# Kernel tuning notes

Measured on AMD Instinct MI355X. Metric: run time of the kernel, lower is better.

The kernel has to match this reference:

```python
import jax, jax.numpy as jnp
import numpy as np

H, D_MODEL, DK, DV = 16, 1024, 64, 64
B, S = 4, 2048
LN_EPS = 1e-6
NEG = -1e9


def setup_inputs() -> dict:
    key = jax.random.key(0)
    ks = jax.random.split(key, 8)
    query = jax.random.normal(ks[0], (B, S, D_MODEL), dtype=jnp.float32)
    k_in = jax.random.normal(ks[1], (B, S, D_MODEL), dtype=jnp.float32)
    v_in = jax.random.normal(ks[2], (B, S, D_MODEL), dtype=jnp.float32)
    mask = jax.random.randint(ks[3], (B, S, S), 0, 2, dtype=jnp.int32)
    sc = 1.0 / np.sqrt(D_MODEL)
    w_qs = jax.random.normal(ks[4], (D_MODEL, H * DK), dtype=jnp.float32) * sc
    w_ks = jax.random.normal(ks[5], (D_MODEL, H * DK), dtype=jnp.float32) * sc
    w_vs = jax.random.normal(ks[6], (D_MODEL, H * DV), dtype=jnp.float32) * sc
    w_out = jax.random.normal(ks[7], (H * DV, D_MODEL), dtype=jnp.float32) * (1.0 / np.sqrt(H * DV))
    ln_g = jnp.ones((D_MODEL,), dtype=jnp.float32)
    ln_b = jnp.zeros((D_MODEL,), dtype=jnp.float32)
    return {"query": query, "key": k_in, "value": v_in, "mask": mask,
            "w_qs": w_qs, "w_ks": w_ks, "w_vs": w_vs, "w_out": w_out,
            "ln_g": ln_g, "ln_b": ln_b}


def reference(query, key, value, mask, w_qs, w_ks, w_vs, w_out, ln_g, ln_b):
    # projections -> [B, H, S, dk/dv]
    q = (query @ w_qs).reshape(B, S, H, DK).transpose(0, 2, 1, 3)
    k = (key @ w_ks).reshape(B, S, H, DK).transpose(0, 2, 1, 3)
    v = (value @ w_vs).reshape(B, S, H, DV).transpose(0, 2, 1, 3)
    scores = jnp.einsum('bhqd,bhkd->bhqk', q, k) / np.sqrt(DK)
    scores = jnp.where(mask[:, None, :, :] == 0, NEG, scores)
    p = jax.nn.softmax(scores, axis=-1)  # dropout = identity in eval
    x = jnp.einsum('bhqk,bhkd->bhqd', p, v)  # [B,H,S,DV]
    x = x.transpose(0, 2, 1, 3).reshape(B, S, H * DV)
    out = x @ w_out + query  # dropout identity, residual
    mu = out.mean(-1, keepdims=True)
    var = out.var(-1, keepdims=True)
    return (out - mu) / jnp.sqrt(var + LN_EPS) * ln_g + ln_b
```

## Files before the change

### kernel.cpp

```cpp
#include <hip/hip_runtime.h>

#define BB   4
#define SS   2048
#define HH   16
#define DM   1024
#define DKV  64
#define LNEPS 1e-6f

#define MD_BF16 0
#define MD_F32  1
#define MD_F16  2

typedef __attribute__((ext_vector_type(8))) short bf16x8;
typedef __attribute__((ext_vector_type(4))) float f32x4;
#define MFMA16(a,b,c) __builtin_amdgcn_mfma_f32_16x16x32_bf16(a,b,c,0,0,0)

__device__ __forceinline__ void gl_lds16(const ushort* g, ushort* l) {
    __builtin_amdgcn_global_load_lds(
        (const __attribute__((address_space(1))) void*)g,
        (__attribute__((address_space(3))) void*)l, 16, 0, 0);
}

__device__ __forceinline__ float2 unpack2(unsigned int u) {
    union { unsigned int i; float f; } a, b;
    a.i = u << 16;
    b.i = u & 0xffff0000u;
    return make_float2(a.f, b.f);
}
__device__ __forceinline__ unsigned short f2bf(float f) {
    union { float f; unsigned int i; } c; c.f = f;
    unsigned int u = c.i;
    unsigned int r = u + 0x7fffu + ((u >> 16) & 1u);
    return (unsigned short)(r >> 16);
}
__device__ __forceinline__ unsigned short f2bf_t(float f) {
    union { float f; unsigned int i; } c; c.f = f;
    return (unsigned short)(c.i >> 16);
}
__device__ __forceinline__ float h2f(unsigned int bits16) {
    unsigned short s = (unsigned short)bits16;
    _Float16 x;
    __builtin_memcpy(&x, &s, 2);
    return (float)x;
}
__device__ __forceinline__ void load8m(const void* p, int mode, size_t e0, float* o) {
    if (mode == MD_F32) {
        const float* f = (const float*)p + e0;
        float4 a = *(const float4*)f;
        float4 b = *(const float4*)(f + 4);
        o[0] = a.x; o[1] = a.y; o[2] = a.z; o[3] = a.w;
        o[4] = b.x; o[5] = b.y; o[6] = b.z; o[7] = b.w;
    } else {
        uint4 u = *(const uint4*)((const ushort*)p + e0);
        unsigned v[4] = {u.x, u.y, u.z, u.w};
        if (mode == MD_BF16) {
#pragma unroll
            for (int j = 0; j < 4; ++j) { float2 t = unpack2(v[j]); o[2*j] = t.x; o[2*j+1] = t.y; }
        } else {
#pragma unroll
            for (int j = 0; j < 4; ++j) { o[2*j] = h2f(v[j] & 0xFFFFu); o[2*j+1] = h2f(v[j] >> 16); }
        }
    }
}
__device__ __forceinline__ void load4m(const void* p, int mode, size_t e0, float* o) {
    if (mode == MD_F32) {
        float4 v = *(const float4*)((const float*)p + e0);
        o[0] = v.x; o[1] = v.y; o[2] = v.z; o[3] = v.w;
    } else {
        uint2 u = *(const uint2*)((const ushort*)p + e0);
        if (mode == MD_BF16) {
            float2 a = unpack2(u.x), b = unpack2(u.y);
            o[0] = a.x; o[1] = a.y; o[2] = b.x; o[3] = b.y;
        } else {
            o[0] = h2f(u.x & 0xFFFFu); o[1] = h2f(u.x >> 16);
            o[2] = h2f(u.y & 0xFFFFu); o[3] = h2f(u.y >> 16);
        }
    }
}
__device__ __forceinline__ float loadS(const void* p, int mode, size_t i) {
    if (mode == MD_F32) return ((const float*)p)[i];
    unsigned short u = ((const ushort*)p)[i];
    if (mode == MD_BF16) { union { unsigned i; float f; } c; c.i = (unsigned)u << 16; return c.f; }
    return h2f(u);
}

struct SniffArgs { const void* p[10]; int nhalf[10]; };

__global__ void sniff_all(SniffArgs a, int* __restrict__ modes) {
    __shared__ int cE, cO;
    const int slots[9] = {0, 1, 2, 4, 5, 6, 7, 8, 9};
    const int slot = slots[blockIdx.x];
    const ushort* p = (const ushort*)a.p[slot];
    const int nhalf = a.nhalf[slot];
    if (threadIdx.x == 0) { cE = 0; cO = 0; }
    __syncthreads();
    int e = 0, o = 0;
    for (int i = threadIdx.x; i < nhalf; i += 256) {
        unsigned ex = (p[i] >> 7) & 0xFFu;
        int hit = (ex < 100u || ex == 0xFFu) ? 1 : 0;
        if (i & 1) o += hit; else e += hit;
    }
    atomicAdd(&cE, e);
    atomicAdd(&cO, o);
    __syncthreads();
    if (threadIdx.x == 0) {
        int total = cE + cO;
        modes[slot] = (total < 48) ? MD_BF16 : ((cO * 4 < cE) ? MD_F32 : MD_F16);
    }
}

__global__ __launch_bounds__(256) void mpack(
    const int* __restrict__ mask, unsigned int* __restrict__ pm)
{
    const int w = blockIdx.x * 256 + threadIdx.x;
    const int* p = mask + (size_t)w * 32;
    unsigned int bits = 0u;
#pragma unroll
    for (int j = 0; j < 8; ++j) {
        int4 v = *(const int4*)(p + j * 4);
        bits |= (v.x ? 1u : 0u) << (4 * j);
        bits |= (v.y ? 1u : 0u) << (4 * j + 1);
        bits |= (v.z ? 1u : 0u) << (4 * j + 2);
        bits |= (v.w ? 1u : 0u) << (4 * j + 3);
    }
    pm[w] = bits;
}

__global__ __launch_bounds__(256) void aconv(
    const void* __restrict__ A, ushort* __restrict__ Ab,
    const int* __restrict__ modes, int slot)
{
    const int m = modes[slot];
    const size_t e0 = ((size_t)blockIdx.x * 256 + threadIdx.x) * 16;
    float t[16];
    load8m(A, m, e0, t);
    load8m(A, m, e0 + 8, t + 8);
    union { ushort u[16]; uint4 v[2]; } p;
#pragma unroll
    for (int j = 0; j < 16; ++j) p.u[j] = f2bf(t[j]);
    *(uint4*)&Ab[e0]     = p.v[0];
    *(uint4*)&Ab[e0 + 8] = p.v[1];
}

__global__ __launch_bounds__(256) void wtrans(
    const void* __restrict__ W, ushort* __restrict__ Wt,
    const int* __restrict__ modes, int wslot)
{
    __shared__ ushort T[64][68];
    const int tid = threadIdx.x;
    const int m = modes[wslot];
    const int k0 = blockIdx.y * 64, n0 = blockIdx.x * 64;

    const int r = tid >> 2, c = (tid & 3) * 16;
    float t[4];
#pragma unroll
    for (int j = 0; j < 4; ++j) {
        load4m(W, m, (size_t)(k0 + r) * DM + n0 + c + 4 * j, t);
#pragma unroll
        for (int i = 0; i < 4; ++i) T[r][c + 4 * j + i] = f2bf(t[i]);
    }
    __syncthreads();

    const int rn = tid >> 2, ck = (tid & 3) * 16;
    union { ushort u[8]; uint4 v; } p0, p1;
#pragma unroll
    for (int j = 0; j < 8; ++j) { p0.u[j] = T[ck + j][rn]; p1.u[j] = T[ck + 8 + j][rn]; }
    ushort* op = &Wt[(size_t)(n0 + rn) * DM + k0 + ck];
    *(uint4*)op = p0.v;
    *(uint4*)(op + 8) = p1.v;
}

__global__ __launch_bounds__(256) void proj_mfma(
    const ushort* __restrict__ A, const ushort* __restrict__ Wt,
    ushort* __restrict__ Out, int vmode, float scale)
{
    __shared__ __align__(16) ushort Asf[128 * 32];
    __shared__ __align__(16) ushort Bsf[128 * 32];

    const int tid = threadIdx.x;
    const int lane = tid & 63, wv = tid >> 6;
    const int quad = lane >> 4, L = lane & 15;
    const int m0 = blockIdx.y * 128, n0 = blockIdx.x * 128;
    const int wm = (wv >> 1) * 64, wn = (wv & 1) * 64;

    const int e0 = (wv * 2 + 0) * 512 + lane * 8;
    const int e1 = (wv * 2 + 1) * 512 + lane * 8;
    const ushort* gA0 = A  + (size_t)(m0 + (e0 >> 5)) * DM + (e0 & 31);
    const ushort* gA1 = A  + (size_t)(m0 + (e1 >> 5)) * DM + (e1 & 31);
    const ushort* gB0 = Wt + (size_t)(n0 + (e0 >> 5)) * DM + (e0 & 31);
    const ushort* gB1 = Wt + (size_t)(n0 + (e1 >> 5)) * DM + (e1 & 31);

    f32x4 acc[4][4];
#pragma unroll
    for (int i = 0; i < 4; ++i)
#pragma unroll
        for (int j = 0; j < 4; ++j) { acc[i][j][0] = 0.f; acc[i][j][1] = 0.f; acc[i][j][2] = 0.f; acc[i][j][3] = 0.f; }

    for (int kt = 0; kt < 32; ++kt) {
        const int k0 = kt * 32;
        gl_lds16(gA0 + k0, &Asf[e0]);
        gl_lds16(gA1 + k0, &Asf[e1]);
        gl_lds16(gB0 + k0, &Bsf[e0]);
        gl_lds16(gB1 + k0, &Bsf[e1]);
        __syncthreads();

        bf16x8 af[4], bfr[4];
#pragma unroll
        for (int tm = 0; tm < 4; ++tm) af[tm] = *(const bf16x8*)&Asf[(wm + tm * 16 + L) * 32 + quad * 8];
#pragma unroll
        for (int tn = 0; tn < 4; ++tn) bfr[tn] = *(const bf16x8*)&Bsf[(wn + tn * 16 + L) * 32 + quad * 8];
#pragma unroll
        for (int tm = 0; tm < 4; ++tm)
#pragma unroll
            for (int tn = 0; tn < 4; ++tn)
                acc[tm][tn] = MFMA16(af[tm], bfr[tn], acc[tm][tn]);
        __syncthreads();
    }

#pragma unroll
    for (int tm = 0; tm < 4; ++tm)
#pragma unroll
        for (int tn = 0; tn < 4; ++tn)
#pragma unroll
            for (int r = 0; r < 4; ++r) {
                const int mm = m0 + wm + tm * 16 + quad * 4 + r;
                const int n = n0 + wn + tn * 16 + L;
                const int b = mm >> 11, s = mm & 2047;
                const int h = n >> 6, d = n & 63;
                const size_t o = vmode
                    ? ((size_t)(b * HH + h) * DKV + d) * SS + s
                    : ((size_t)(b * HH + h) * SS + s) * DKV + d;
                Out[o] = f2bf(acc[tm][tn][r] * scale);
            }
}

__global__ __launch_bounds__(256) void attn_mfma(
    const ushort* __restrict__ Q, const ushort* __restrict__ K,
    const ushort* __restrict__ Vt, const unsigned int* __restrict__ pm,
    ushort* __restrict__ Xo)
{
    __shared__ __align__(16) ushort Ks[64][72];
    __shared__ __align__(16) ushort Vs[64][72];
    __shared__ __align__(16) ushort Ps[64][72];

    const int tid = threadIdx.x;
    const int lane = tid & 63, wv = tid >> 6;
    const int quad = lane >> 4, L = lane & 15;
    const int bh = blockIdx.y, b = bh >> 4, h = bh & 15;
    const int q0 = blockIdx.x * 64;

    const ushort* qp = &Q[((size_t)bh * SS + q0 + wv * 16 + L) * DKV + quad * 8];
    const bf16x8 aq0 = *(const bf16x8*)qp;
    const bf16x8 aq1 = *(const bf16x8*)(qp + 32);

    f32x4 O[4];
    float lacc[4];
#pragma unroll
    for (int t = 0; t < 4; ++t) { O[t][0] = 0.f; O[t][1] = 0.f; O[t][2] = 0.f; O[t][3] = 0.f; }
#pragma unroll
    for (int r = 0; r < 4; ++r) lacc[r] = 0.f;

    const int sr = tid >> 2, sg = tid & 3;
    const ushort* kbase = &K[((size_t)bh * SS + sr) * DKV + sg * 16];
    const ushort* vbase = &Vt[((size_t)bh * DKV + sr) * SS + sg * 16];
    const unsigned int* pmr[4];
#pragma unroll
    for (int r = 0; r < 4; ++r)
        pmr[r] = pm + ((size_t)b * SS + q0 + wv * 16 + quad * 4 + r) * 64;

    for (int kt = 0; kt < 32; ++kt) {
        __syncthreads();
        *(uint4*)&Ks[sr][sg * 16]     = *(const uint4*)kbase;
        *(uint4*)&Ks[sr][sg * 16 + 8] = *(const uint4*)(kbase + 8);
        *(uint4*)&Vs[sr][sg * 16]     = *(const uint4*)vbase;
        *(uint4*)&Vs[sr][sg * 16 + 8] = *(const uint4*)(vbase + 8);
        kbase += 64 * DKV;
        vbase += 64;

        uint2 mw[4];
#pragma unroll
        for (int r = 0; r < 4; ++r) mw[r] = *(const uint2*)(pmr[r] + 2 * kt);

        __syncthreads();

        f32x4 sc[4];
#pragma unroll
        for (int t = 0; t < 4; ++t) {
            bf16x8 b0 = *(const bf16x8*)&Ks[t * 16 + L][quad * 8];
            bf16x8 b1 = *(const bf16x8*)&Ks[t * 16 + L][32 + quad * 8];
            f32x4 c; c[0] = 0.f; c[1] = 0.f; c[2] = 0.f; c[3] = 0.f;
            c = MFMA16(aq0, b0, c);
            c = MFMA16(aq1, b1, c);
            sc[t] = c;
        }

#pragma unroll
        for (int r = 0; r < 4; ++r) {
            const unsigned mx = mw[r].x, my = mw[r].y;
#pragma unroll
            for (int t = 0; t < 4; ++t) {
                const float s = fminf(sc[t][r], 30.f);
                const float e = __expf(s);
                const unsigned wsel = (t & 2) ? my : mx;
                const float p = ((wsel >> ((t & 1) * 16 + L)) & 1u) ? e : 0.f;
                lacc[r] += p;
                Ps[wv * 16 + quad * 4 + r][t * 16 + L] = f2bf_t(p);
            }
        }

        bf16x8 ap0 = *(const bf16x8*)&Ps[wv * 16 + L][quad * 8];
        bf16x8 ap1 = *(const bf16x8*)&Ps[wv * 16 + L][32 + quad * 8];
#pragma unroll
        for (int t = 0; t < 4; ++t) {
            bf16x8 v0 = *(const bf16x8*)&Vs[t * 16 + L][quad * 8];
            bf16x8 v1 = *(const bf16x8*)&Vs[t * 16 + L][32 + quad * 8];
            O[t] = MFMA16(ap0, v0, O[t]);
            O[t] = MFMA16(ap1, v1, O[t]);
        }
    }

    float inv[4];
#pragma unroll
    for (int r = 0; r < 4; ++r) {
        float l = lacc[r];
#pragma unroll
        for (int off = 1; off < 16; off <<= 1) l += __shfl_xor(l, off, 64);
        inv[r] = 1.f / l;
    }
#pragma unroll
    for (int t = 0; t < 4; ++t)
#pragma unroll
        for (int r = 0; r < 4; ++r) {
            const int qg = q0 + wv * 16 + quad * 4 + r;
            Xo[((size_t)b * SS + qg) * DM + h * DKV + t * 16 + L] = f2bf(O[t][r] * inv[r]);
        }
}

__global__ __launch_bounds__(256) void oproj_mfma(
    const ushort* __restrict__ Xin, const ushort* __restrict__ Wt,
    const void* __restrict__ Qres, float* __restrict__ Out,
    const int* __restrict__ modes)
{
    __shared__ __align__(16) ushort Asf[128 * 32];
    __shared__ __align__(16) ushort Bsf[128 * 32];

    const int tid = threadIdx.x;
    const int lane = tid & 63, wv = tid >> 6;
    const int quad = lane >> 4, L = lane & 15;
    const int m0 = blockIdx.y * 128, n0 = blockIdx.x * 128;
    const int wm = (wv >> 1) * 64, wn = (wv & 1) * 64;
    const int mq = modes[0];

    const int e0 = (wv * 2 + 0) * 512 + lane * 8;
    const int e1 = (wv * 2 + 1) * 512 + lane * 8;
    const ushort* gA0 = Xin + (size_t)(m0 + (e0 >> 5)) * DM + (e0 & 31);
    const ushort* gA1 = Xin + (size_t)(m0 + (e1 >> 5)) * DM + (e1 & 31);
    const ushort* gB0 = Wt  + (size_t)(n0 + (e0 >> 5)) * DM + (e0 & 31);
    const ushort* gB1 = Wt  + (size_t)(n0 + (e1 >> 5)) * DM + (e1 & 31);

    f32x4 acc[4][4];
#pragma unroll
    for (int i = 0; i < 4; ++i)
#pragma unroll
        for (int j = 0; j < 4; ++j) { acc[i][j][0] = 0.f; acc[i][j][1] = 0.f; acc[i][j][2] = 0.f; acc[i][j][3] = 0.f; }

    for (int kt = 0; kt < 32; ++kt) {
        const int k0 = kt * 32;
        gl_lds16(gA0 + k0, &Asf[e0]);
        gl_lds16(gA1 + k0, &Asf[e1]);
        gl_lds16(gB0 + k0, &Bsf[e0]);
        gl_lds16(gB1 + k0, &Bsf[e1]);
        __syncthreads();

        bf16x8 af[4], bfr[4];
#pragma unroll
        for (int tm = 0; tm < 4; ++tm) af[tm] = *(const bf16x8*)&Asf[(wm + tm * 16 + L) * 32 + quad * 8];
#pragma unroll
        for (int tn = 0; tn < 4; ++tn) bfr[tn] = *(const bf16x8*)&Bsf[(wn + tn * 16 + L) * 32 + quad * 8];
#pragma unroll
        for (int tm = 0; tm < 4; ++tm)
#pragma unroll
            for (int tn = 0; tn < 4; ++tn)
                acc[tm][tn] = MFMA16(af[tm], bfr[tn], acc[tm][tn]);
        __syncthreads();
    }

#pragma unroll
    for (int tm = 0; tm < 4; ++tm)
#pragma unroll
        for (int tn = 0; tn < 4; ++tn)
#pragma unroll
            for (int r = 0; r < 4; ++r) {
                const int mm = m0 + wm + tm * 16 + quad * 4 + r;
                const int n = n0 + wn + tn * 16 + L;
                const size_t idx = (size_t)mm * DM + n;
                Out[idx] = acc[tm][tn][r] + loadS(Qres, mq, idx);
            }
}

__global__ __launch_bounds__(256) void ln_k(
    float* __restrict__ Out, const void* __restrict__ G,
    const void* __restrict__ Bt, const int* __restrict__ modes)
{
    const int tid = threadIdx.x, wv = tid >> 6, lane = tid & 63;
    const int row = blockIdx.x * 4 + wv;
    const int mg = modes[8], mb = modes[9];
    const size_t base = (size_t)row * DM + lane * 16;

    float v[16];
    float s = 0.f, q = 0.f;
#pragma unroll
    for (int j = 0; j < 16; j += 4) {
        float4 t = *(const float4*)&Out[base + j];
        v[j] = t.x; v[j+1] = t.y; v[j+2] = t.z; v[j+3] = t.w;
        s += t.x + t.y + t.z + t.w;
        q += t.x*t.x + t.y*t.y + t.z*t.z + t.w*t.w;
    }
#pragma unroll
    for (int off = 1; off < 64; off <<= 1) {
        s += __shfl_xor(s, off, 64);
        q += __shfl_xor(q, off, 64);
    }
    const float mu = s * (1.f / 1024.f);
    const float var = q * (1.f / 1024.f) - mu * mu;
    const float inv = rsqrtf(var + LNEPS);

    float gj[16], bj[16];
#pragma unroll
    for (int j = 0; j < 16; j += 4) {
        load4m(G,  mg, (size_t)lane * 16 + j, gj + j);
        load4m(Bt, mb, (size_t)lane * 16 + j, bj + j);
    }
#pragma unroll
    for (int j = 0; j < 16; j += 4) {
        float4 o;
        o.x = (v[j]   - mu) * inv * gj[j]   + bj[j];
        o.y = (v[j+1] - mu) * inv * gj[j+1] + bj[j+1];
        o.z = (v[j+2] - mu) * inv * gj[j+2] + bj[j+2];
        o.w = (v[j+3] - mu) * inv * gj[j+3] + bj[j+3];
        *(float4*)&Out[base + j] = o;
    }
}

extern "C" void kernel_launch(void* const* d_in, const int* in_sizes, int n_in,
                              void* d_out, int out_size, void* d_ws, size_t ws_size,
                              hipStream_t stream)
{
    const void* query = d_in[0];
    const void* key_i = d_in[1];
    const void* value = d_in[2];
    const int*  mask  = (const int*)d_in[3];
    const void* w_qs  = d_in[4];
    const void* w_ks  = d_in[5];
    const void* w_vs  = d_in[6];
    const void* w_out = d_in[7];
    const void* ln_g  = d_in[8];
    const void* ln_b  = d_in[9];
    float* out = (float*)d_out;

    int* modes = (int*)d_ws;
    const size_t PE = (size_t)BB * HH * SS * DKV;
    ushort* Qw = (ushort*)((char*)d_ws + 256);
    ushort* Kw = Qw + PE;
    ushort* Vw = Kw + PE;
    ushort* Xw = Vw + PE;
    ushort* Abuf = Xw;
    ushort* Wt   = (ushort*)((char*)d_out + (4 << 20));
    ushort* Wt2  = Qw;
    unsigned int* pmask = (unsigned int*)d_out;

    SniffArgs sa;
    for (int i = 0; i < 10; ++i) {
        sa.p[i] = d_in[i];
        sa.nhalf[i] = in_sizes[i] < 4096 ? in_sizes[i] : 4096;
    }
    sniff_all<<<9, 256, 0, stream>>>(sa, modes);
    mpack<<<2048, 256, 0, stream>>>(mask, pmask);

    dim3 gproj(8, 64), gtr(16, 16);

    wtrans<<<gtr, 256, 0, stream>>>(w_qs, Wt, modes, 4);
    aconv<<<2048, 256, 0, stream>>>(query, Abuf, modes, 0);
    proj_mfma<<<gproj, 256, 0, stream>>>(Abuf, Wt, Qw, 0, 0.125f);

    wtrans<<<gtr, 256, 0, stream>>>(w_ks, Wt, modes, 5);
    aconv<<<2048, 256, 0, stream>>>(key_i, Abuf, modes, 1);
    proj_mfma<<<gproj, 256, 0, stream>>>(Abuf, Wt, Kw, 0, 1.0f);

    wtrans<<<gtr, 256, 0, stream>>>(w_vs, Wt, modes, 6);
    aconv<<<2048, 256, 0, stream>>>(value, Abuf, modes, 2);
    proj_mfma<<<gproj, 256, 0, stream>>>(Abuf, Wt, Vw, 1, 1.0f);

    attn_mfma<<<dim3(32, 64), 256, 0, stream>>>(Qw, Kw, Vw, pmask, Xw);

    wtrans<<<gtr, 256, 0, stream>>>(w_out, Wt2, modes, 7);
    oproj_mfma<<<gproj, 256, 0, stream>>>(Xw, Wt2, query, out, modes);
    ln_k<<<2048, 256, 0, stream>>>(out, ln_g, ln_b, modes);
}
```

Measured before the change: 536.4 us.

## Double-buffer GEMM LDS loads, swizzle block order, batch weight transposes, set MFMA priority

The projection and output GEMMs now use double-buffered LDS tiles. The next k-slice's global_load_lds is issued before the MFMAs on the current slice, and each step ends with a single vmcnt wait plus barrier. This is meant to hide global-load latency. Block indices are swizzled in the GEMMs and in attention, so consecutive blocks share tiles in L2. The three QKV weight transposes are merged into one launch writing separate buffers, and s_setprio is raised around the MFMA sections in attention. The cost is double the LDS per GEMM block, which may reduce occupancy.

```diff
diff --git a/kernel.cpp b/kernel.cpp
--- a/kernel.cpp
+++ b/kernel.cpp
@@ -19,6 +19,10 @@
     __builtin_amdgcn_global_load_lds(
         (const __attribute__((address_space(1))) void*)g,
         (__attribute__((address_space(3))) void*)l, 16, 0, 0);
+}
+__device__ __forceinline__ void wait_vm0_barrier() {
+    asm volatile("s_waitcnt vmcnt(0)" ::: "memory");
+    __builtin_amdgcn_s_barrier();
 }
 
 __device__ __forceinline__ float2 unpack2(unsigned int u) {
@@ -142,13 +146,13 @@
     *(uint4*)&Ab[e0 + 8] = p.v[1];
 }
 
-__global__ __launch_bounds__(256) void wtrans(
-    const void* __restrict__ W, ushort* __restrict__ Wt,
-    const int* __restrict__ modes, int wslot)
+struct WtArgs { const void* W[3]; ushort* Wt[3]; int slot[3]; };
+
+__device__ __forceinline__ void wtrans_body(
+    const void* __restrict__ W, ushort* __restrict__ Wt, int m)
 {
     __shared__ ushort T[64][68];
     const int tid = threadIdx.x;
-    const int m = modes[wslot];
     const int k0 = blockIdx.y * 64, n0 = blockIdx.x * 64;
 
     const int r = tid >> 2, c = (tid & 3) * 16;
@@ -170,17 +174,30 @@
     *(uint4*)(op + 8) = p1.v;
 }
 
+__global__ __launch_bounds__(256) void wtrans3(WtArgs a, const int* __restrict__ modes) {
+    const int g = blockIdx.z;
+    wtrans_body(a.W[g], a.Wt[g], modes[a.slot[g]]);
+}
+__global__ __launch_bounds__(256) void wtrans(
+    const void* __restrict__ W, ushort* __restrict__ Wt,
+    const int* __restrict__ modes, int wslot)
+{
+    wtrans_body(W, Wt, modes[wslot]);
+}
+
 __global__ __launch_bounds__(256) void proj_mfma(
     const ushort* __restrict__ A, const ushort* __restrict__ Wt,
     ushort* __restrict__ Out, int vmode, float scale)
 {
-    __shared__ __align__(16) ushort Asf[128 * 32];
-    __shared__ __align__(16) ushort Bsf[128 * 32];
+    __shared__ __align__(16) ushort Asf[2][4096];
+    __shared__ __align__(16) ushort Bsf[2][4096];
 
     const int tid = threadIdx.x;
     const int lane = tid & 63, wv = tid >> 6;
     const int quad = lane >> 4, L = lane & 15;
-    const int m0 = blockIdx.y * 128, n0 = blockIdx.x * 128;
+    const int bid = blockIdx.y * gridDim.x + blockIdx.x;
+    const int swz = (bid & 7) * 64 + (bid >> 3);
+    const int m0 = (swz >> 3) * 128, n0 = (swz & 7) * 128;
     const int wm = (wv >> 1) * 64, wn = (wv & 1) * 64;
 
     const int e0 = (wv * 2 + 0) * 512 + lane * 8;
@@ -196,25 +213,45 @@
 #pragma unroll
         for (int j = 0; j < 4; ++j) { acc[i][j][0] = 0.f; acc[i][j][1] = 0.f; acc[i][j][2] = 0.f; acc[i][j][3] = 0.f; }
 
-    for (int kt = 0; kt < 32; ++kt) {
-        const int k0 = kt * 32;
-        gl_lds16(gA0 + k0, &Asf[e0]);
-        gl_lds16(gA1 + k0, &Asf[e1]);
-        gl_lds16(gB0 + k0, &Bsf[e0]);
-        gl_lds16(gB1 + k0, &Bsf[e1]);
-        __syncthreads();
+    gl_lds16(gA0, &Asf[0][e0]);
+    gl_lds16(gA1, &Asf[0][e1]);
+    gl_lds16(gB0, &Bsf[0][e0]);
+    gl_lds16(gB1, &Bsf[0][e1]);
+    wait_vm0_barrier();
+
+    int cur = 0;
+    for (int kt = 0; kt < 31; ++kt) {
+        const int kn = (kt + 1) * 32;
+        gl_lds16(gA0 + kn, &Asf[cur ^ 1][e0]);
+        gl_lds16(gA1 + kn, &Asf[cur ^ 1][e1]);
+        gl_lds16(gB0 + kn, &Bsf[cur ^ 1][e0]);
+        gl_lds16(gB1 + kn, &Bsf[cur ^ 1][e1]);
 
         bf16x8 af[4], bfr[4];
 #pragma unroll
-        for (int tm = 0; tm < 4; ++tm) af[tm] = *(const bf16x8*)&Asf[(wm + tm * 16 + L) * 32 + quad * 8];
-#pragma unroll
-        for (int tn = 0; tn < 4; ++tn) bfr[tn] = *(const bf16x8*)&Bsf[(wn + tn * 16 + L) * 32 + quad * 8];
+        for (int tm = 0; tm < 4; ++tm) af[tm] = *(const bf16x8*)&Asf[cur][(wm + tm * 16 + L) * 32 + quad * 8];
+#pragma unroll
+        for (int tn = 0; tn < 4; ++tn) bfr[tn] = *(const bf16x8*)&Bsf[cur][(wn + tn * 16 + L) * 32 + quad * 8];
 #pragma unroll
         for (int tm = 0; tm < 4; ++tm)
 #pragma unroll
             for (int tn = 0; tn < 4; ++tn)
                 acc[tm][tn] = MFMA16(af[tm], bfr[tn], acc[tm][tn]);
-        __syncthreads();
+
+        wait_vm0_barrier();
+        cur ^= 1;
+    }
+    {
+        bf16x8 af[4], bfr[4];
+#pragma unroll
+        for (int tm = 0; tm < 4; ++tm) af[tm] = *(const bf16x8*)&Asf[cur][(wm + tm * 16 + L) * 32 + quad * 8];
+#pragma unroll
+        for (int tn = 0; tn < 4; ++tn) bfr[tn] = *(const bf16x8*)&Bsf[cur][(wn + tn * 16 + L) * 32 + quad * 8];
+#pragma unroll
+        for (int tm = 0; tm < 4; ++tm)
+#pragma unroll
+            for (int tn = 0; tn < 4; ++tn)
+                acc[tm][tn] = MFMA16(af[tm], bfr[tn], acc[tm][tn]);
     }
 
 #pragma unroll
@@ -246,8 +283,10 @@
     const int tid = threadIdx.x;
     const int lane = tid & 63, wv = tid >> 6;
     const int quad = lane >> 4, L = lane & 15;
-    const int bh = blockIdx.y, b = bh >> 4, h = bh & 15;
-    const int q0 = blockIdx.x * 64;
+    const int bid = blockIdx.y * gridDim.x + blockIdx.x;
+    const int swz = (bid & 7) * 256 + (bid >> 3);
+    const int bh = swz >> 5, b = bh >> 4, h = bh & 15;
+    const int q0 = (swz & 31) * 64;
 
     const ushort* qp = &Q[((size_t)bh * SS + q0 + wv * 16 + L) * DKV + quad * 8];
     const bf16x8 aq0 = *(const bf16x8*)qp;
@@ -284,6 +323,7 @@
         __syncthreads();
 
         f32x4 sc[4];
+        __builtin_amdgcn_s_setprio(1);
 #pragma unroll
         for (int t = 0; t < 4; ++t) {
             bf16x8 b0 = *(const bf16x8*)&Ks[t * 16 + L][quad * 8];
@@ -293,6 +333,7 @@
             c = MFMA16(aq1, b1, c);
             sc[t] = c;
         }
+        __builtin_amdgcn_s_setprio(0);
 
 #pragma unroll
         for (int r = 0; r < 4; ++r) {
@@ -310,6 +351,7 @@
 
         bf16x8 ap0 = *(const bf16x8*)&Ps[wv * 16 + L][quad * 8];
         bf16x8 ap1 = *(const bf16x8*)&Ps[wv * 16 + L][32 + quad * 8];
+        __builtin_amdgcn_s_setprio(1);
 #pragma unroll
         for (int t = 0; t < 4; ++t) {
             bf16x8 v0 = *(const bf16x8*)&Vs[t * 16 + L][quad * 8];
@@ -317,6 +359,7 @@
             O[t] = MFMA16(ap0, v0, O[t]);
             O[t] = MFMA16(ap1, v1, O[t]);
         }
+        __builtin_amdgcn_s_setprio(0);
     }
 
     float inv[4];
@@ -341,13 +384,15 @@
     const void* __restrict__ Qres, float* __restrict__ Out,
     const int* __restrict__ modes)
 {
-    __shared__ __align__(16) ushort Asf[128 * 32];
-    __shared__ __align__(16) ushort Bsf[128 * 32];
+    __shared__ __align__(16) ushort Asf[2][4096];
+    __shared__ __align__(16) ushort Bsf[2][4096];
 
     const int tid = threadIdx.x;
     const int lane = tid & 63, wv = tid >> 6;
     const int quad = lane >> 4, L = lane & 15;
-    const int m0 = blockIdx.y * 128, n0 = blockIdx.x * 128;
+    const int bid = blockIdx.y * gridDim.x + blockIdx.x;
+    const int swz = (bid & 7) * 64 + (bid >> 3);
+    const int m0 = (swz >> 3) * 128, n0 = (swz & 7) * 128;
     const int wm = (wv >> 1) * 64, wn = (wv & 1) * 64;
     const int mq = modes[0];
 
@@ -364,25 +409,45 @@
 #pragma unroll
         for (int j = 0; j < 4; ++j) { acc[i][j][0] = 0.f; acc[i][j][1] = 0.f; acc[i][j][2] = 0.f; acc[i][j][3] = 0.f; }
 
-    for (int kt = 0; kt < 32; ++kt) {
-        const int k0 = kt * 32;
-        gl_lds16(gA0 + k0, &Asf[e0]);
-        gl_lds16(gA1 + k0, &Asf[e1]);
-        gl_lds16(gB0 + k0, &Bsf[e0]);
-        gl_lds16(gB1 + k0, &Bsf[e1]);
-        __syncthreads();
+    gl_lds16(gA0, &Asf[0][e0]);
+    gl_lds16(gA1, &Asf[0][e1]);
+    gl_lds16(gB0, &Bsf[0][e0]);
+    gl_lds16(gB1, &Bsf[0][e1]);
+    wait_vm0_barrier();
+
+    int cur = 0;
+    for (int kt = 0; kt < 31; ++kt) {
+        const int kn = (kt + 1) * 32;
+        gl_lds16(gA0 + kn, &Asf[cur ^ 1][e0]);
+        gl_lds16(gA1 + kn, &Asf[cur ^ 1][e1]);
+        gl_lds16(gB0 + kn, &Bsf[cur ^ 1][e0]);
+        gl_lds16(gB1 + kn, &Bsf[cur ^ 1][e1]);
 
         bf16x8 af[4], bfr[4];
 #pragma unroll
-        for (int tm = 0; tm < 4; ++tm) af[tm] = *(const bf16x8*)&Asf[(wm + tm * 16 + L) * 32 + quad * 8];
-#pragma unroll
-        for (int tn = 0; tn < 4; ++tn) bfr[tn] = *(const bf16x8*)&Bsf[(wn + tn * 16 + L) * 32 + quad * 8];
+        for (int tm = 0; tm < 4; ++tm) af[tm] = *(const bf16x8*)&Asf[cur][(wm + tm * 16 + L) * 32 + quad * 8];
+#pragma unroll
+        for (int tn = 0; tn < 4; ++tn) bfr[tn] = *(const bf16x8*)&Bsf[cur][(wn + tn * 16 + L) * 32 + quad * 8];
 #pragma unroll
         for (int tm = 0; tm < 4; ++tm)
 #pragma unroll
             for (int tn = 0; tn < 4; ++tn)
                 acc[tm][tn] = MFMA16(af[tm], bfr[tn], acc[tm][tn]);
-        __syncthreads();
+
+        wait_vm0_barrier();
+        cur ^= 1;
+    }
+    {
+        bf16x8 af[4], bfr[4];
+#pragma unroll
+        for (int tm = 0; tm < 4; ++tm) af[tm] = *(const bf16x8*)&Asf[cur][(wm + tm * 16 + L) * 32 + quad * 8];
+#pragma unroll
+        for (int tn = 0; tn < 4; ++tn) bfr[tn] = *(const bf16x8*)&Bsf[cur][(wn + tn * 16 + L) * 32 + quad * 8];
+#pragma unroll
+        for (int tm = 0; tm < 4; ++tm)
+#pragma unroll
+            for (int tn = 0; tn < 4; ++tn)
+                acc[tm][tn] = MFMA16(af[tm], bfr[tn], acc[tm][tn]);
     }
 
 #pragma unroll
@@ -465,7 +530,9 @@
     ushort* Vw = Kw + PE;
     ushort* Xw = Vw + PE;
     ushort* Abuf = Xw;
-    ushort* Wt   = (ushort*)((char*)d_out + (4 << 20));
+    ushort* Wtq  = (ushort*)((char*)d_out + (4  << 20));
+    ushort* Wtk  = (ushort*)((char*)d_out + (8  << 20));
+    ushort* Wtv  = (ushort*)((char*)d_out + (12 << 20));
     ushort* Wt2  = Qw;
     unsigned int* pmask = (unsigned int*)d_out;
 
@@ -477,19 +544,22 @@
     sniff_all<<<9, 256, 0, stream>>>(sa, modes);
     mpack<<<2048, 256, 0, stream>>>(mask, pmask);
 
+    WtArgs wa;
+    wa.W[0] = w_qs; wa.Wt[0] = Wtq; wa.slot[0] = 4;
+    wa.W[1] = w_ks; wa.Wt[1] = Wtk; wa.slot[1] = 5;
+    wa.W[2] = w_vs; wa.Wt[2] = Wtv; wa.slot[2] = 6;
+    wtrans3<<<dim3(16, 16, 3), 256, 0, stream>>>(wa, modes);
+
     dim3 gproj(8, 64), gtr(16, 16);
 
-    wtrans<<<gtr, 256, 0, stream>>>(w_qs, Wt, modes, 4);
     aconv<<<2048, 256, 0, stream>>>(query, Abuf, modes, 0);
-    proj_mfma<<<gproj, 256, 0, stream>>>(Abuf, Wt, Qw, 0, 0.125f);
-
-    wtrans<<<gtr, 256, 0, stream>>>(w_ks, Wt, modes, 5);
+    proj_mfma<<<gproj, 256, 0, stream>>>(Abuf, Wtq, Qw, 0, 0.125f);
+
     aconv<<<2048, 256, 0, stream>>>(key_i, Abuf, modes, 1);
-    proj_mfma<<<gproj, 256, 0, stream>>>(Abuf, Wt, Kw, 0, 1.0f);
-
-    wtrans<<<gtr, 256, 0, stream>>>(w_vs, Wt, modes, 6);
+    proj_mfma<<<gproj, 256, 0, stream>>>(Abuf, Wtk, Kw, 0, 1.0f);
+
     aconv<<<2048, 256, 0, stream>>>(value, Abuf, modes, 2);
-    proj_mfma<<<gproj, 256, 0, stream>>>(Abuf, Wt, Vw, 1, 1.0f);
+    proj_mfma<<<gproj, 256, 0, stream>>>(Abuf, Wtv, Vw, 1, 1.0f);
 
     attn_mfma<<<dim3(32, 64), 256, 0, stream>>>(Qw, Kw, Vw, pmask, Xw);
 
```

Result: no change. 527.1 us (-1.7%).
